# Performance work log

Hardware: AMD Instinct MI355X
Metric: run time of the kernel (lower is better)

Reference implementation:

```python
import jax, jax.numpy as jnp
import numpy as np

D_MODEL = 1024
HEADS = 16
Q_DIM = 1024
HEAD_DIM = Q_DIM // HEADS


def setup_inputs() -> dict:
    key = jax.random.key(0)
    ks = jax.random.split(key, 9)
    B, S = 2, 2048
    scale = 1.0 / np.sqrt(D_MODEL)
    inp = {
        "embeddings": jax.random.normal(ks[0], (B, S, D_MODEL), dtype=jnp.float32),
        "Wq": jax.random.normal(ks[1], (D_MODEL, Q_DIM), dtype=jnp.float32) * scale,
        "bq": jnp.zeros((Q_DIM,), dtype=jnp.float32),
        "Wk": jax.random.normal(ks[2], (D_MODEL, Q_DIM), dtype=jnp.float32) * scale,
        "bk": jnp.zeros((Q_DIM,), dtype=jnp.float32),
        "Wv": jax.random.normal(ks[3], (D_MODEL, Q_DIM), dtype=jnp.float32) * scale,
        "bv": jnp.zeros((Q_DIM,), dtype=jnp.float32),
        "Wo": jax.random.normal(ks[4], (Q_DIM, D_MODEL), dtype=jnp.float32) * scale,
        "bo": jnp.zeros((D_MODEL,), dtype=jnp.float32),
    }
    return inp


def reference(embeddings, Wq, bq, Wk, bk, Wv, bv, Wo, bo):
    B, S, _ = embeddings.shape
    # projections -> [B, H, S, Dh]
    def proj(W, b):
        x = embeddings @ W + b
        return x.reshape(B, S, HEADS, HEAD_DIM).transpose(0, 2, 1, 3)
    q = proj(Wq, bq)
    k = proj(Wk, bk)
    v = proj(Wv, bv)
    # scores scaled by sqrt(head_dim) as in source (no mask, dropout is no-op)
    scores = jnp.einsum("bhqd,bhkd->bhqk", q, k) / jnp.sqrt(
        jnp.asarray(HEAD_DIM, dtype=q.dtype)
    )
    p = jax.nn.softmax(scores, axis=-1)
    attn = jnp.einsum("bhqk,bhkd->bhqd", p, v)
    attn = attn.transpose(0, 2, 1, 3).reshape(B, S, Q_DIM)
    return attn @ Wo + bo
```

## Files before the change

### kernel.cpp

```cpp
#include <hip/hip_runtime.h>
#include <hip/hip_bf16.h>

#define BB 2
#define SS 2048
#define DMODEL 1024
#define NHEADS 16
#define DHEAD 64
#define MTOT (BB*SS)
#define NQKV 3072
#define QSCALE 0.18033688011112042f

typedef short bh8 __attribute__((ext_vector_type(8)));
typedef float fx4 __attribute__((ext_vector_type(4)));

__device__ __forceinline__ short f2bs(float f) {
    __hip_bfloat16 h = __float2bfloat16(f);
    return *reinterpret_cast<short*>(&h);
}

__device__ __forceinline__ void gload_lds16(const short* g, short* l) {
    __builtin_amdgcn_global_load_lds(
        (const __attribute__((address_space(1))) unsigned int*)g,
        (__attribute__((address_space(3))) unsigned int*)l, 16, 0, 0);
}

__global__ __launch_bounds__(256) void cvt_emb(const float* __restrict__ x,
                                               short* __restrict__ y, int n) {
    int i = (blockIdx.x * 256 + threadIdx.x) * 4;
    if (i + 3 < n) {
        float4 v = *(const float4*)(x + i);
        short4 o;
        o.x = f2bs(v.x); o.y = f2bs(v.y); o.z = f2bs(v.z); o.w = f2bs(v.w);
        *(short4*)(y + i) = o;
    }
}

__global__ __launch_bounds__(256) void transpose_w(
        const float* __restrict__ Wq, const float* __restrict__ Wk,
        const float* __restrict__ Wv, const float* __restrict__ Wo,
        short* __restrict__ Wt_qkv, short* __restrict__ Wot) {
    __shared__ float tile[64][65];
    int z = blockIdx.z;
    const float* src = (z == 0) ? Wq : (z == 1) ? Wk : (z == 2) ? Wv : Wo;
    short* dst = (z == 3) ? Wot : (Wt_qkv + (size_t)z * 1024 * 1024);
    int n0 = blockIdx.x * 64, k0 = blockIdx.y * 64;
    int tx = threadIdx.x, ty = threadIdx.y;
    for (int j = 0; j < 16; j++) {
        int r = ty + j * 4;
        tile[r][tx] = src[(size_t)(k0 + r) * 1024 + n0 + tx];
    }
    __syncthreads();
    for (int j = 0; j < 16; j++) {
        int r = ty + j * 4;
        dst[(size_t)(n0 + r) * 1024 + k0 + tx] = f2bs(tile[tx][r]);
    }
}

template<int BM, int BN, int NN, int MODE>
__global__ __launch_bounds__(256) void gemm_bt_t(
        const short* __restrict__ A, const short* __restrict__ Bt,
        const float* __restrict__ bq, const float* __restrict__ bk,
        const float* __restrict__ bv, const float* __restrict__ bo,
        short* __restrict__ Qout, short* __restrict__ Kout,
        short* __restrict__ Vtout, float* __restrict__ Cout) {
    const int K = 1024;
    constexpr int ROWS = BM + BN;
    constexpr int CPW  = ROWS / 64;
    constexpr int MBK  = MTOT / BM;
    constexpr int STRIP = MBK / 8;
    constexpr int MT = BM / 32, NT = BN / 32;
    __shared__ __align__(16) short S[3][ROWS * 32];

    int tid = threadIdx.x;
    int w = tid >> 6, l = tid & 63, quad = l >> 4, ln = l & 15;
    int wm = w & 1, wn = w >> 1;

    int id = blockIdx.x;
    int xcd = id & 7, local = id >> 3;
    int mi = xcd * STRIP + (local % STRIP);
    int ni = local / STRIP;
    int m0 = mi * BM, n0 = ni * BN;

    const short* gsrc[CPW];
    int loff[CPW];
    #pragma unroll
    for (int j = 0; j < CPW; j++) {
        int r0 = (w * CPW + j) * 16;
        int row = r0 + (l >> 2);
        gsrc[j] = (r0 < BM ? A + (size_t)(m0 + row) * K
                           : Bt + (size_t)(n0 + row - BM) * K) + (l & 3) * 8;
        loff[j] = r0 * 32;
    }

    short *sC = &S[0][0], *sN = &S[1][0], *sN2 = &S[2][0];
    #pragma unroll
    for (int j = 0; j < CPW; j++) gload_lds16(gsrc[j], sC + loff[j]);
    #pragma unroll
    for (int j = 0; j < CPW; j++) gload_lds16(gsrc[j] + 32, sN + loff[j]);

    fx4 acc[MT][NT] = {};
    for (int it = 0; it < 32; ++it) {
        if (it < 31) {
            if constexpr (CPW == 4)
                asm volatile("s_waitcnt vmcnt(4)\n\ts_barrier" ::: "memory");
            else
                asm volatile("s_waitcnt vmcnt(3)\n\ts_barrier" ::: "memory");
        } else {
            asm volatile("s_waitcnt vmcnt(0)\n\ts_barrier" ::: "memory");
        }
        if (it < 30) {
            int k0 = (it + 2) * 32;
            #pragma unroll
            for (int j = 0; j < CPW; j++) gload_lds16(gsrc[j] + k0, sN2 + loff[j]);
        }
        bh8 af[MT], bf[NT];
        #pragma unroll
        for (int mt = 0; mt < MT; mt++)
            af[mt] = *(const bh8*)&sC[(wm * (BM / 2) + mt * 16 + ln) * 32 + quad * 8];
        #pragma unroll
        for (int nt = 0; nt < NT; nt++)
            bf[nt] = *(const bh8*)&sC[(BM + wn * (BN / 2) + nt * 16 + ln) * 32 + quad * 8];
        #pragma unroll
        for (int mt = 0; mt < MT; mt++)
            #pragma unroll
            for (int nt = 0; nt < NT; nt++)
                acc[mt][nt] = __builtin_amdgcn_mfma_f32_16x16x32_bf16(af[mt], bf[nt], acc[mt][nt], 0, 0, 0);
        short* t;
        t = sC; sC = sN; sN = sN2; sN2 = t;
    }

    #pragma unroll
    for (int mt = 0; mt < MT; mt++) {
        #pragma unroll
        for (int nt = 0; nt < NT; nt++) {
            int n = n0 + wn * (BN / 2) + nt * 16 + ln;
            int mbase = m0 + wm * (BM / 2) + mt * 16 + quad * 4;
            #pragma unroll
            for (int r = 0; r < 4; r++) {
                float v = acc[mt][nt][r];
                int m = mbase + r;
                if constexpr (MODE == 0) {
                    int which = n >> 10, nn = n & 1023, h = nn >> 6, d = nn & 63;
                    float bias = (which == 0) ? bq[nn] : (which == 1) ? bk[nn] : bv[nn];
                    v += bias;
                    int b = m >> 11, s = m & 2047;
                    if (which == 0)
                        Qout[(((size_t)(b * 16 + h) * 2048) + s) * 64 + d] = f2bs(v * QSCALE);
                    else if (which == 1)
                        Kout[(((size_t)(b * 16 + h) * 2048) + s) * 64 + d] = f2bs(v);
                    else
                        Vtout[((size_t)(b * 16 + h) * 64 + d) * 2048 + s] = f2bs(v);
                } else {
                    Cout[(size_t)m * 1024 + n] = v + bo[n];
                }
            }
        }
    }
}

__global__ __launch_bounds__(256, 4) void flash_attn(
        const short* __restrict__ Q, const short* __restrict__ Kg,
        const short* __restrict__ Vt,
        float* __restrict__ O0, float* __restrict__ O1,
        float* __restrict__ L0, float* __restrict__ L1) {
    __shared__ __align__(16) short Ks[64 * 64];
    __shared__ __align__(16) short Vs[64 * 64];
    __shared__ __align__(16) short Ps[4][32 * 68];

    int tid = threadIdx.x;
    int w = tid >> 6, l = tid & 63, quad = l >> 4, ln = l & 15;
    int id = blockIdx.x;
    int xcd = id & 7, local = id >> 3;
    int bh = xcd * 4 + (local & 3);
    int t = local >> 2;
    int qx = t & 15, z = t >> 4;
    int qblk = qx * 128 + w * 32;
    const short* Qb = Q  + (size_t)bh * 2048 * 64;
    const short* Kb = Kg + (size_t)bh * 2048 * 64 + (size_t)z * 1024 * 64;
    const short* Vb = Vt + (size_t)bh * 64 * 2048 + z * 1024;
    float* Op = z ? O1 : O0;
    float* Lp = z ? L1 : L0;
    int swz = ln & 7;

    bh8 qf[2][2];
    #pragma unroll
    for (int qt = 0; qt < 2; qt++)
        #pragma unroll
        for (int c = 0; c < 2; c++)
            qf[qt][c] = *(const bh8*)&Qb[(size_t)(qblk + qt * 16 + ln) * 64 + c * 32 + quad * 8];

    int srow = tid >> 2, sp0 = tid & 3;
    int kw0 = srow * 64 + ((sp0 ^ (srow & 7)) * 8);
    int kw1 = srow * 64 + (((sp0 + 4) ^ (srow & 7)) * 8);
    const short* gK = Kb + (size_t)srow * 64;
    const short* gV = Vb + (size_t)srow * 2048;

    {
        uint4 a = *(const uint4*)(gK + sp0 * 8);
        uint4 bb = *(const uint4*)(gK + (sp0 + 4) * 8);
        uint4 c = *(const uint4*)(gV + sp0 * 8);
        uint4 d = *(const uint4*)(gV + (sp0 + 4) * 8);
        *(uint4*)&Ks[kw0] = a; *(uint4*)&Ks[kw1] = bb;
        *(uint4*)&Vs[kw0] = c; *(uint4*)&Vs[kw1] = d;
    }
    asm volatile("s_waitcnt lgkmcnt(0)\n\ts_barrier" ::: "memory");

    fx4 o[2][4] = {};
    float lpart[2] = {0.f, 0.f};

    for (int it = 0; it < 16; ++it) {
        uint4 ra, rb, rc, rd;
        bool pre = (it < 15);
        if (pre) {
            const short* gk = gK + (size_t)(it + 1) * 4096;
            const short* gv = gV + (size_t)(it + 1) * 64;
            ra = *(const uint4*)(gk + sp0 * 8);
            rb = *(const uint4*)(gk + (sp0 + 4) * 8);
            rc = *(const uint4*)(gv + sp0 * 8);
            rd = *(const uint4*)(gv + (sp0 + 4) * 8);
        }

        fx4 s[2][4] = {};
        #pragma unroll
        for (int mt = 0; mt < 4; mt++) {
            bh8 kf0 = *(const bh8*)&Ks[(mt * 16 + ln) * 64 + ((quad ^ swz) * 8)];
            bh8 kf1 = *(const bh8*)&Ks[(mt * 16 + ln) * 64 + (((quad + 4) ^ swz) * 8)];
            #pragma unroll
            for (int qt = 0; qt < 2; qt++) {
                s[qt][mt] = __builtin_amdgcn_mfma_f32_16x16x32_bf16(kf0, qf[qt][0], s[qt][mt], 0, 0, 0);
                s[qt][mt] = __builtin_amdgcn_mfma_f32_16x16x32_bf16(kf1, qf[qt][1], s[qt][mt], 0, 0, 0);
            }
        }

        #pragma unroll
        for (int qt = 0; qt < 2; qt++) {
            #pragma unroll
            for (int mt = 0; mt < 4; mt++) {
                float p0 = __builtin_amdgcn_exp2f(s[qt][mt][0]);
                float p1 = __builtin_amdgcn_exp2f(s[qt][mt][1]);
                float p2 = __builtin_amdgcn_exp2f(s[qt][mt][2]);
                float p3 = __builtin_amdgcn_exp2f(s[qt][mt][3]);
                lpart[qt] += (p0 + p1) + (p2 + p3);
                union { __hip_bfloat162 h2[2]; short4 s4; } u;
                u.h2[0] = __float22bfloat162_rn(make_float2(p0, p1));
                u.h2[1] = __float22bfloat162_rn(make_float2(p2, p3));
                *(short4*)&Ps[w][(qt * 16 + ln) * 64 +
                                 (((mt * 2 + (quad >> 1)) ^ swz) * 8) + (quad & 1) * 4] = u.s4;
            }
        }
        asm volatile("s_waitcnt lgkmcnt(0)" ::: "memory");

        #pragma unroll
        for (int c2 = 0; c2 < 2; c2++) {
            bh8 pf0 = *(const bh8*)&Ps[w][(0 * 16 + ln) * 64 + (((c2 * 4 + quad) ^ swz) * 8)];
            bh8 pf1 = *(const bh8*)&Ps[w][(1 * 16 + ln) * 64 + (((c2 * 4 + quad) ^ swz) * 8)];
            #pragma unroll
            for (int dt = 0; dt < 4; dt++) {
                bh8 vf = *(const bh8*)&Vs[(dt * 16 + ln) * 64 + (((c2 * 4 + quad) ^ swz) * 8)];
                o[0][dt] = __builtin_amdgcn_mfma_f32_16x16x32_bf16(vf, pf0, o[0][dt], 0, 0, 0);
                o[1][dt] = __builtin_amdgcn_mfma_f32_16x16x32_bf16(vf, pf1, o[1][dt], 0, 0, 0);
            }
        }

        asm volatile("s_barrier" ::: "memory");
        if (pre) {
            *(uint4*)&Ks[kw0] = ra; *(uint4*)&Ks[kw1] = rb;
            *(uint4*)&Vs[kw0] = rc; *(uint4*)&Vs[kw1] = rd;
        }
        asm volatile("s_waitcnt lgkmcnt(0)\n\ts_barrier" ::: "memory");
    }

    float* PsF = (float*)&Ps[w][0];
    int row = l >> 2, seg = l & 3;
    #pragma unroll
    for (int qt = 0; qt < 2; qt++) {
        #pragma unroll
        for (int dt = 0; dt < 4; dt++)
            *(fx4*)&PsF[ln * 68 + dt * 16 + quad * 4] = o[qt][dt];
        asm volatile("s_waitcnt lgkmcnt(0)" ::: "memory");
        float* orow = &Op[((size_t)bh * 2048 + qblk + qt * 16 + row) * 64];
        #pragma unroll
        for (int j = 0; j < 4; j++) {
            fx4 v = *(fx4*)&PsF[row * 68 + seg * 16 + j * 4];
            *(fx4*)&orow[seg * 16 + j * 4] = v;
        }
        asm volatile("s_waitcnt lgkmcnt(0)" ::: "memory");
        float lr = lpart[qt];
        lr += __shfl_xor(lr, 16);
        lr += __shfl_xor(lr, 32);
        if (l < 16) Lp[(size_t)bh * 2048 + qblk + qt * 16 + l] = lr;
    }
}

__global__ __launch_bounds__(256) void combine(
        const float* __restrict__ O0, const float* __restrict__ O1,
        const float* __restrict__ L0, const float* __restrict__ L1,
        short* __restrict__ Ctx) {
    int t = blockIdx.x * 256 + threadIdx.x;
    size_t base = (size_t)t * 8;
    int bhq = t >> 3;
    int d = (t & 7) * 8;
    int bh = bhq >> 11, q = bhq & 2047;
    int b = bh >> 4, h = bh & 15;
    float inv = 1.0f / (L0[bhq] + L1[bhq]);
    float4 a0 = *(const float4*)(O0 + base);
    float4 a1 = *(const float4*)(O0 + base + 4);
    float4 c0 = *(const float4*)(O1 + base);
    float4 c1 = *(const float4*)(O1 + base + 4);
    union { short s[8]; bh8 v; } o;
    o.s[0] = f2bs((a0.x + c0.x) * inv); o.s[1] = f2bs((a0.y + c0.y) * inv);
    o.s[2] = f2bs((a0.z + c0.z) * inv); o.s[3] = f2bs((a0.w + c0.w) * inv);
    o.s[4] = f2bs((a1.x + c1.x) * inv); o.s[5] = f2bs((a1.y + c1.y) * inv);
    o.s[6] = f2bs((a1.z + c1.z) * inv); o.s[7] = f2bs((a1.w + c1.w) * inv);
    *(bh8*)&Ctx[((size_t)(b * 2048 + q)) * 1024 + h * 64 + d] = o.v;
}

extern "C" void kernel_launch(void* const* d_in, const int* in_sizes, int n_in,
                              void* d_out, int out_size, void* d_ws, size_t ws_size,
                              hipStream_t stream) {
    const float* emb = (const float*)d_in[0];
    const float* Wq  = (const float*)d_in[1];
    const float* bq  = (const float*)d_in[2];
    const float* Wk  = (const float*)d_in[3];
    const float* bk  = (const float*)d_in[4];
    const float* Wv  = (const float*)d_in[5];
    const float* bv  = (const float*)d_in[6];
    const float* Wo  = (const float*)d_in[7];
    const float* bo  = (const float*)d_in[8];

    char* ws = (char*)d_ws;
    const size_t MB = 1024 * 1024;
    short* Xbf  = (short*)(ws + 0);
    short* Wt   = (short*)(ws + 8 * MB);
    float* Op1  = (float*)(ws + 0);
    short* Wot  = (short*)(ws + 17 * MB);
    short* Qb   = (short*)(ws + 19 * MB);
    short* Ctx  = (short*)(ws + 19 * MB);
    short* Kb   = (short*)(ws + 27 * MB);
    short* Vtb  = (short*)(ws + 35 * MB);
    float* L0   = (float*)(ws + 43 * MB);
    float* L1   = (float*)(ws + 43 * MB + 256 * 1024);
    float* Op0  = (float*)d_out;

    cvt_emb<<<4096, 256, 0, stream>>>(emb, Xbf, MTOT * DMODEL);
    transpose_w<<<dim3(16, 16, 4), dim3(64, 4), 0, stream>>>(Wq, Wk, Wv, Wo, Wt, Wot);
    gemm_bt_t<128, 128, NQKV, 0><<<768, 256, 0, stream>>>(
        Xbf, Wt, bq, bk, bv, nullptr, Qb, Kb, Vtb, nullptr);
    flash_attn<<<1024, 256, 0, stream>>>(Qb, Kb, Vtb, Op0, Op1, L0, L1);
    combine<<<2048, 256, 0, stream>>>(Op0, Op1, L0, L1, Ctx);
    gemm_bt_t<64, 128, DMODEL, 1><<<512, 256, 0, stream>>>(
        Ctx, Wot, nullptr, nullptr, nullptr, bo, nullptr, nullptr, nullptr, (float*)d_out);
}
```

Measured before the change: 210.9 us.

## Double-buffer K/V via direct global-to-LDS loads and keep P in registers

```diff
diff --git a/kernel.cpp b/kernel.cpp
--- a/kernel.cpp
+++ b/kernel.cpp
@@ -12,10 +12,16 @@
 
 typedef short bh8 __attribute__((ext_vector_type(8)));
 typedef float fx4 __attribute__((ext_vector_type(4)));
+typedef unsigned int ux2 __attribute__((ext_vector_type(2)));
 
 __device__ __forceinline__ short f2bs(float f) {
     __hip_bfloat16 h = __float2bfloat16(f);
     return *reinterpret_cast<short*>(&h);
+}
+
+__device__ __forceinline__ unsigned pk_bf16(float a, float b) {
+    __hip_bfloat162 h = __float22bfloat162_rn(make_float2(a, b));
+    return *reinterpret_cast<unsigned*>(&h);
 }
 
 __device__ __forceinline__ void gload_lds16(const short* g, short* l) {
@@ -163,9 +169,7 @@
         const short* __restrict__ Vt,
         float* __restrict__ O0, float* __restrict__ O1,
         float* __restrict__ L0, float* __restrict__ L1) {
-    __shared__ __align__(16) short Ks[64 * 64];
-    __shared__ __align__(16) short Vs[64 * 64];
-    __shared__ __align__(16) short Ps[4][32 * 68];
+    __shared__ __align__(16) short SH[16384];
 
     int tid = threadIdx.x;
     int w = tid >> 6, l = tid & 63, quad = l >> 4, ln = l & 15;
@@ -189,42 +193,46 @@
         for (int c = 0; c < 2; c++)
             qf[qt][c] = *(const bh8*)&Qb[(size_t)(qblk + qt * 16 + ln) * 64 + c * 32 + quad * 8];
 
-    int srow = tid >> 2, sp0 = tid & 3;
-    int kw0 = srow * 64 + ((sp0 ^ (srow & 7)) * 8);
-    int kw1 = srow * 64 + (((sp0 + 4) ^ (srow & 7)) * 8);
-    const short* gK = Kb + (size_t)srow * 64;
-    const short* gV = Vb + (size_t)srow * 2048;
-
-    {
-        uint4 a = *(const uint4*)(gK + sp0 * 8);
-        uint4 bb = *(const uint4*)(gK + (sp0 + 4) * 8);
-        uint4 c = *(const uint4*)(gV + sp0 * 8);
-        uint4 d = *(const uint4*)(gV + (sp0 + 4) * 8);
-        *(uint4*)&Ks[kw0] = a; *(uint4*)&Ks[kw1] = bb;
-        *(uint4*)&Vs[kw0] = c; *(uint4*)&Vs[kw1] = d;
-    }
-    asm volatile("s_waitcnt lgkmcnt(0)\n\ts_barrier" ::: "memory");
+    const short* srcK[2]; const short* srcV[2]; int dstoff[2];
+    #pragma unroll
+    for (int j = 0; j < 2; j++) {
+        int c = w * 2 + j;
+        int row = c * 8 + (l >> 3);
+        int pg = (l & 7) ^ (row & 7);
+        srcK[j] = Kb + row * 64 + pg * 8;
+        srcV[j] = Vb + (size_t)row * 2048 + pg * 8;
+        dstoff[j] = c * 512;
+    }
+
+    #pragma unroll
+    for (int j = 0; j < 2; j++) {
+        gload_lds16(srcK[j], SH + dstoff[j]);
+        gload_lds16(srcV[j], SH + 8192 + dstoff[j]);
+    }
 
     fx4 o[2][4] = {};
     float lpart[2] = {0.f, 0.f};
 
     for (int it = 0; it < 16; ++it) {
-        uint4 ra, rb, rc, rd;
-        bool pre = (it < 15);
-        if (pre) {
-            const short* gk = gK + (size_t)(it + 1) * 4096;
-            const short* gv = gV + (size_t)(it + 1) * 64;
-            ra = *(const uint4*)(gk + sp0 * 8);
-            rb = *(const uint4*)(gk + (sp0 + 4) * 8);
-            rc = *(const uint4*)(gv + sp0 * 8);
-            rd = *(const uint4*)(gv + (sp0 + 4) * 8);
-        }
+        int koff = (it & 1) ? 4096 : 0;
+        asm volatile("s_waitcnt vmcnt(0) lgkmcnt(0)\n\ts_barrier" ::: "memory");
+        if (it < 15) {
+            int noff = koff ^ 4096;
+            int kg = (it + 1) * 4096, vg = (it + 1) * 64;
+            #pragma unroll
+            for (int j = 0; j < 2; j++) {
+                gload_lds16(srcK[j] + kg, SH + noff + dstoff[j]);
+                gload_lds16(srcV[j] + vg, SH + 8192 + noff + dstoff[j]);
+            }
+        }
+        const short* ksb = SH + koff;
+        const short* vsb = SH + 8192 + koff;
 
         fx4 s[2][4] = {};
         #pragma unroll
         for (int mt = 0; mt < 4; mt++) {
-            bh8 kf0 = *(const bh8*)&Ks[(mt * 16 + ln) * 64 + ((quad ^ swz) * 8)];
-            bh8 kf1 = *(const bh8*)&Ks[(mt * 16 + ln) * 64 + (((quad + 4) ^ swz) * 8)];
+            bh8 kf0 = *(const bh8*)&ksb[(mt * 16 + ln) * 64 + ((quad ^ swz) * 8)];
+            bh8 kf1 = *(const bh8*)&ksb[(mt * 16 + ln) * 64 + (((quad + 4) ^ swz) * 8)];
             #pragma unroll
             for (int qt = 0; qt < 2; qt++) {
                 s[qt][mt] = __builtin_amdgcn_mfma_f32_16x16x32_bf16(kf0, qf[qt][0], s[qt][mt], 0, 0, 0);
@@ -232,45 +240,48 @@
             }
         }
 
+        bh8 pf[2][2];
         #pragma unroll
         for (int qt = 0; qt < 2; qt++) {
+            float e[4][4];
             #pragma unroll
             for (int mt = 0; mt < 4; mt++) {
-                float p0 = __builtin_amdgcn_exp2f(s[qt][mt][0]);
-                float p1 = __builtin_amdgcn_exp2f(s[qt][mt][1]);
-                float p2 = __builtin_amdgcn_exp2f(s[qt][mt][2]);
-                float p3 = __builtin_amdgcn_exp2f(s[qt][mt][3]);
-                lpart[qt] += (p0 + p1) + (p2 + p3);
-                union { __hip_bfloat162 h2[2]; short4 s4; } u;
-                u.h2[0] = __float22bfloat162_rn(make_float2(p0, p1));
-                u.h2[1] = __float22bfloat162_rn(make_float2(p2, p3));
-                *(short4*)&Ps[w][(qt * 16 + ln) * 64 +
-                                 (((mt * 2 + (quad >> 1)) ^ swz) * 8) + (quad & 1) * 4] = u.s4;
-            }
-        }
-        asm volatile("s_waitcnt lgkmcnt(0)" ::: "memory");
+                #pragma unroll
+                for (int r = 0; r < 4; r++)
+                    e[mt][r] = __builtin_amdgcn_exp2f(s[qt][mt][r]);
+                lpart[qt] += (e[mt][0] + e[mt][1]) + (e[mt][2] + e[mt][3]);
+            }
+            #pragma unroll
+            for (int c2 = 0; c2 < 2; c2++) {
+                unsigned xa = pk_bf16(e[2 * c2][0], e[2 * c2][1]);
+                unsigned ya = pk_bf16(e[2 * c2][2], e[2 * c2][3]);
+                unsigned xb = pk_bf16(e[2 * c2 + 1][0], e[2 * c2 + 1][1]);
+                unsigned yb = pk_bf16(e[2 * c2 + 1][2], e[2 * c2 + 1][3]);
+                ux2 u  = __builtin_amdgcn_permlane32_swap(xa, xb, false, false);
+                ux2 d02 = __builtin_amdgcn_permlane16_swap(u.x, u.y, false, false);
+                ux2 u2 = __builtin_amdgcn_permlane32_swap(ya, yb, false, false);
+                ux2 d13 = __builtin_amdgcn_permlane16_swap(u2.x, u2.y, false, false);
+                union { unsigned u4[4]; bh8 v; } pk_;
+                pk_.u4[0] = d02.x; pk_.u4[1] = d13.x;
+                pk_.u4[2] = d02.y; pk_.u4[3] = d13.y;
+                pf[qt][c2] = pk_.v;
+            }
+        }
 
         #pragma unroll
         for (int c2 = 0; c2 < 2; c2++) {
-            bh8 pf0 = *(const bh8*)&Ps[w][(0 * 16 + ln) * 64 + (((c2 * 4 + quad) ^ swz) * 8)];
-            bh8 pf1 = *(const bh8*)&Ps[w][(1 * 16 + ln) * 64 + (((c2 * 4 + quad) ^ swz) * 8)];
             #pragma unroll
             for (int dt = 0; dt < 4; dt++) {
-                bh8 vf = *(const bh8*)&Vs[(dt * 16 + ln) * 64 + (((c2 * 4 + quad) ^ swz) * 8)];
-                o[0][dt] = __builtin_amdgcn_mfma_f32_16x16x32_bf16(vf, pf0, o[0][dt], 0, 0, 0);
-                o[1][dt] = __builtin_amdgcn_mfma_f32_16x16x32_bf16(vf, pf1, o[1][dt], 0, 0, 0);
-            }
-        }
-
-        asm volatile("s_barrier" ::: "memory");
-        if (pre) {
-            *(uint4*)&Ks[kw0] = ra; *(uint4*)&Ks[kw1] = rb;
-            *(uint4*)&Vs[kw0] = rc; *(uint4*)&Vs[kw1] = rd;
-        }
-        asm volatile("s_waitcnt lgkmcnt(0)\n\ts_barrier" ::: "memory");
-    }
-
-    float* PsF = (float*)&Ps[w][0];
+                bh8 vf = *(const bh8*)&vsb[(dt * 16 + ln) * 64 + (((c2 * 4 + quad) ^ swz) * 8)];
+                o[0][dt] = __builtin_amdgcn_mfma_f32_16x16x32_bf16(vf, pf[0][c2], o[0][dt], 0, 0, 0);
+                o[1][dt] = __builtin_amdgcn_mfma_f32_16x16x32_bf16(vf, pf[1][c2], o[1][dt], 0, 0, 0);
+            }
+        }
+    }
+
+    asm volatile("s_waitcnt lgkmcnt(0)\n\ts_barrier" ::: "memory");
+
+    float* PsF = (float*)SH + w * 1088;
     int row = l >> 2, seg = l & 3;
     #pragma unroll
     for (int qt = 0; qt < 2; qt++) {
```

Result: no change. 208.6 us (-1.1%).
